# Optimization experiments

Measured on AMD Instinct MI355X. Metric: run time of the kernel, lower is better.

Reference implementation:

```python
import jax, jax.numpy as jnp
import numpy as np

B, L, D, H = 4, 2048, 2048, 16
HEAD_DIM = D // H
EPS = 1e-5


def rmsnorm(x, w):
    # fp32 RMSNorm as in the torch module
    xf = x.astype(jnp.float32)
    rms = jnp.sqrt(jnp.mean(xf * xf, axis=-1, keepdims=True) + EPS)
    return xf / rms * w


def apply_rope(x, freqs):
    # x: (..., D) with interleaved even/odd pairs; freqs: (2, L, D/2) = (sin, cos)
    sin, cos = freqs[0], freqs[1]
    xr = x.reshape(*x.shape[:-1], D // 2, 2)
    x_even, x_odd = xr[..., 0], xr[..., 1]
    e = x_even * cos - x_odd * sin
    o = x_odd * cos + x_even * sin
    return jnp.stack([e, o], axis=-1).reshape(x.shape)


def setup_inputs() -> dict:
    key = jax.random.key(0)
    k0, k1, k2 = jax.random.split(key, 3)
    x_BLD = jax.random.normal(k0, (B, L, D), dtype=jnp.float32)
    # realistic RoPE angle table over the full dim (matches module usage)
    t = jnp.arange(L, dtype=jnp.float32)[:, None]
    inv_freq = 1.0 / (10000.0 ** (jnp.arange(D // 2, dtype=jnp.float32) / (D // 2)))
    ang = t * inv_freq[None, :]                      # (L, D/2)
    freqs = jnp.stack([jnp.sin(ang), jnp.cos(ang)])  # (2, L, D/2)
    wqkv = jax.random.normal(k1, (3 * D, D), dtype=jnp.float32) * 0.02
    wo = jax.random.normal(k2, (D, D), dtype=jnp.float32) * 0.02
    q_norm_w = jnp.ones((D,), dtype=jnp.float32)
    k_norm_w = jnp.ones((D,), dtype=jnp.float32)
    return {"x_BLD": x_BLD, "freqs": freqs, "wqkv": wqkv, "wo": wo,
            "q_norm_w": q_norm_w, "k_norm_w": k_norm_w}


def reference(x_BLD, freqs, wqkv, wo, q_norm_w, k_norm_w):
    dtype = x_BLD.dtype
    qkv = x_BLD @ wqkv.T                             # (B, L, 3D)
    q, k, v = jnp.split(qkv, 3, axis=-1)
    q = apply_rope(rmsnorm(q, q_norm_w), freqs).astype(dtype)
    k = apply_rope(rmsnorm(k, k_norm_w), freqs).astype(dtype)
    # (B, L, D) -> (B, H, L, hd)
    q = q.reshape(B, L, H, HEAD_DIM).transpose(0, 2, 1, 3)
    k = k.reshape(B, L, H, HEAD_DIM).transpose(0, 2, 1, 3)
    v = v.reshape(B, L, H, HEAD_DIM).transpose(0, 2, 1, 3)
    scale = HEAD_DIM ** -0.5
    scores = jnp.einsum('bhqd,bhkd->bhqk', q, k) * scale
    attn = jax.nn.softmax(scores, axis=-1)
    out = jnp.einsum('bhqk,bhkd->bhqd', attn, v)
    out = out.transpose(0, 2, 1, 3).reshape(B, L, D)
    return out @ wo.T
```

## Files before the change

### kernel.cpp

```cpp
#include <hip/hip_runtime.h>
#include <stdint.h>
#include <stddef.h>

typedef unsigned short u16;
typedef __bf16 bf16x8 __attribute__((ext_vector_type(8)));
typedef float  f32x4  __attribute__((ext_vector_type(4)));
typedef float  f32x16 __attribute__((ext_vector_type(16)));

__device__ __forceinline__ float bf2f(u16 u){ return __uint_as_float(((unsigned)u)<<16); }
__device__ __forceinline__ u16 f2bf(float f){
  unsigned u = __float_as_uint(f);
  return (u16)((u + 0x7fffu + ((u>>16)&1u)) >> 16);
}
__device__ __forceinline__ void gl_lds16(const void* g, void* s){
  __builtin_amdgcn_global_load_lds(
      (__attribute__((address_space(1))) void*)(void*)g,
      (__attribute__((address_space(3))) void*)s, 16, 0, 0);
}

__global__ void k_f2bf(const float* __restrict__ in, u16* __restrict__ out, int n4){
  int i = blockIdx.x*256 + threadIdx.x;
  if (i < n4){
    float4 v = ((const float4*)in)[i];
    ((ushort4*)out)[i] = make_ushort4(f2bf(v.x), f2bf(v.y), f2bf(v.z), f2bf(v.w));
  }
}

#define BAR()  do{ __asm__ __volatile__("" ::: "memory"); \
                   __builtin_amdgcn_s_barrier(); \
                   __asm__ __volatile__("" ::: "memory"); }while(0)
#define LGKM0() __asm__ __volatile__("s_waitcnt lgkmcnt(0)" ::: "memory")
#define VMC4()  __asm__ __volatile__("s_waitcnt vmcnt(4)" ::: "memory")
#define VMC0()  __asm__ __volatile__("s_waitcnt vmcnt(0)" ::: "memory")

#define STAGE_A(B_,H_,T_) do{ \
  const u16* _s = A + (size_t)(m0 + (H_)*128 + w16 + sr)*K + (T_)*64 + sc; \
  gl_lds16(_s,               &As[B_][H_][w16*64]); \
  gl_lds16(_s + (size_t)8*K, &As[B_][H_][(w16+8)*64]); }while(0)
#define STAGE_B(B_,H_,T_) do{ \
  const u16* _s = Bm + (size_t)(n0 + (H_)*128 + w16 + sr)*K + (T_)*64 + sc; \
  gl_lds16(_s,               &Bs[B_][H_][w16*64]); \
  gl_lds16(_s + (size_t)8*K, &Bs[B_][H_][(w16+8)*64]); }while(0)

#define RD_A(H_,B_) do{ \
  _Pragma("unroll") for (int mt=0; mt<4; ++mt){ \
    int r_ = wm*64 + mt*16 + l16; const u16* p_ = &As[B_][H_][r_*64]; \
    af[mt][0] = *(const bf16x8*)&p_[(( quad    ^ (r_&7))<<3)]; \
    af[mt][1] = *(const bf16x8*)&p_[(((quad+4) ^ (r_&7))<<3)]; } }while(0)
#define RD_B(H_,B_) do{ \
  _Pragma("unroll") for (int nt=0; nt<2; ++nt){ \
    int r_ = wn*32 + nt*16 + l16; const u16* p_ = &Bs[B_][H_][r_*64]; \
    bfr[nt][0] = *(const bf16x8*)&p_[(( quad    ^ (r_&7))<<3)]; \
    bfr[nt][1] = *(const bf16x8*)&p_[(((quad+4) ^ (r_&7))<<3)]; } }while(0)

#define MM(QM,QN) do{ \
  LGKM0(); \
  __builtin_amdgcn_s_setprio(1); \
  _Pragma("unroll") for (int k_=0;k_<2;++k_) \
    _Pragma("unroll") for (int mt=0;mt<4;++mt) \
      _Pragma("unroll") for (int nt=0;nt<2;++nt) \
        acc[QM][QN][mt][nt] = __builtin_amdgcn_mfma_f32_16x16x32_bf16( \
            af[mt][k_], bfr[nt][k_], acc[QM][QN][mt][nt], 0,0,0); \
  __builtin_amdgcn_s_setprio(0); }while(0)

template<int BF16OUT>
__global__ __launch_bounds__(512,2) void k_gemm256(const u16* __restrict__ A,
                                                   const u16* __restrict__ Bm,
                                                   void* __restrict__ Cout,
                                                   int M, int N, int K){
  __shared__ __align__(16) u16 As[2][2][128*64];
  __shared__ __align__(16) u16 Bs[2][2][128*64];
  const int tid = threadIdx.x, w = tid>>6, ln = tid&63;
  const int l16 = ln&15, quad = ln>>4;
  const int wm = w&1, wn = w>>1;
  const int w16 = w*16, sr = ln>>3;
  const int sc = ((ln&7) ^ sr) << 3;
  const int nbx = N>>8;
  const int nwg = nbx*(M>>8);
  const int lid = blockIdx.y*nbx + blockIdx.x;
  const int swz = (lid&7)*(nwg>>3) + (lid>>3);
  const int m0 = (swz/nbx)<<8, n0 = (swz%nbx)<<8;

  f32x4 acc[2][2][4][2];
  #pragma unroll
  for (int a=0;a<2;++a)
    #pragma unroll
    for (int b=0;b<2;++b)
      #pragma unroll
      for (int c=0;c<4;++c)
        #pragma unroll
        for (int d=0;d<2;++d){ acc[a][b][c][d][0]=0.f; acc[a][b][c][d][1]=0.f;
                               acc[a][b][c][d][2]=0.f; acc[a][b][c][d][3]=0.f; }
  bf16x8 af[4][2], bfr[2][2];

  STAGE_A(0,0,0); STAGE_B(0,0,0); STAGE_A(0,1,0); STAGE_B(0,1,0);
  STAGE_B(1,0,1); STAGE_A(1,1,1);
  VMC4(); BAR();

  const int niter = K>>7;
  for (int j=0; j<niter-1; ++j){
    const int t1 = 2*j+1;
    RD_A(0,0); RD_B(0,0); STAGE_A(1,0,t1);           BAR(); MM(0,0); BAR();
    RD_A(1,0);            STAGE_B(1,1,t1);           BAR(); MM(1,0); BAR();
    RD_B(1,0);            STAGE_B(0,0,t1+1);         BAR(); MM(1,1); BAR();
    RD_A(0,0);            STAGE_A(0,1,t1+1); VMC4(); BAR(); MM(0,1); BAR();
    RD_A(0,1); RD_B(0,1); STAGE_A(0,0,t1+1);         BAR(); MM(0,0); BAR();
    RD_A(1,1);            STAGE_B(0,1,t1+1);         BAR(); MM(1,0); BAR();
    RD_B(1,1);            STAGE_B(1,0,t1+2);         BAR(); MM(1,1); BAR();
    RD_A(0,1);            STAGE_A(1,1,t1+2); VMC4(); BAR(); MM(0,1); BAR();
  }
  {
    const int T1 = 2*niter-1;
    RD_A(0,0); RD_B(0,0); STAGE_A(1,0,T1);           BAR(); MM(0,0); BAR();
    RD_A(1,0);            STAGE_B(1,1,T1);           BAR(); MM(1,0); BAR();
    RD_B(1,0);                                       BAR(); MM(1,1); BAR();
    RD_A(0,0);                               VMC0(); BAR(); MM(0,1); BAR();
    RD_A(0,1); RD_B(0,1);                            BAR(); MM(0,0); BAR();
    RD_A(1,1);                                       BAR(); MM(1,0); BAR();
    RD_B(1,1);                                       BAR(); MM(1,1); BAR();
    RD_A(0,1);                                       BAR(); MM(0,1); BAR();
  }
  #pragma unroll
  for (int qm=0;qm<2;++qm)
    #pragma unroll
    for (int qn=0;qn<2;++qn)
      #pragma unroll
      for (int mt=0;mt<4;++mt)
        #pragma unroll
        for (int nt=0;nt<2;++nt)
          #pragma unroll
          for (int jj=0;jj<4;++jj){
            int row = m0 + qm*128 + wm*64 + mt*16 + quad*4 + jj;
            int col = n0 + qn*128 + wn*32 + nt*16 + l16;
            if (BF16OUT) ((u16*)Cout)[(size_t)row*N + col] = f2bf(acc[qm][qn][mt][nt][jj]);
            else         ((float*)Cout)[(size_t)row*N + col] = acc[qm][qn][mt][nt][jj];
          }
}

__global__ void k_prep_qk(const u16* __restrict__ qkv, const float* __restrict__ freqs,
                          const float* __restrict__ qw, const float* __restrict__ kw,
                          u16* __restrict__ Qo, u16* __restrict__ Ko){
  const int row = blockIdx.x;
  const int b = row >> 11, l = row & 2047;
  const int tid = threadIdx.x;
  const u16* qr = qkv + (size_t)row*6144;
  float qe[4], qo[4], ke[4], ko_[4];
  float sq = 0.f, sk = 0.f;
  #pragma unroll
  for (int it=0; it<4; ++it){
    int p = tid + it*256;
    ushort2 q2 = ((const ushort2*)qr)[p];
    ushort2 k2 = ((const ushort2*)(qr+2048))[p];
    qe[it]=bf2f(q2.x); qo[it]=bf2f(q2.y);
    ke[it]=bf2f(k2.x); ko_[it]=bf2f(k2.y);
    sq += qe[it]*qe[it] + qo[it]*qo[it];
    sk += ke[it]*ke[it] + ko_[it]*ko_[it];
  }
  #pragma unroll
  for (int off=32; off; off>>=1){ sq += __shfl_xor(sq, off); sk += __shfl_xor(sk, off); }
  __shared__ float red[8];
  if ((tid&63)==0){ red[tid>>6]=sq; red[4+(tid>>6)]=sk; }
  __syncthreads();
  sq = red[0]+red[1]+red[2]+red[3];
  sk = red[4]+red[5]+red[6]+red[7];
  const float rq = rsqrtf(sq*(1.f/2048.f) + 1e-5f);
  const float rk = rsqrtf(sk*(1.f/2048.f) + 1e-5f);
  const float QS = 0.08838834764831845f * 1.4426950408889634f;
  #pragma unroll
  for (int it=0; it<4; ++it){
    int p = tid + it*256;
    float sn = freqs[(size_t)l*1024 + p];
    float cs = freqs[2097152 + (size_t)l*1024 + p];
    float2 w2q = ((const float2*)qw)[p];
    float2 w2k = ((const float2*)kw)[p];
    int h = p>>6, dd2 = p&63;
    size_t o = ((size_t)(b*16+h)*2048 + l)*64 + dd2;
    float a = qe[it]*rq*w2q.x, c = qo[it]*rq*w2q.y;
    ((ushort2*)Qo)[o] = make_ushort2(f2bf((a*cs - c*sn)*QS), f2bf((c*cs + a*sn)*QS));
    a = ke[it]*rk*w2k.x; c = ko_[it]*rk*w2k.y;
    ((ushort2*)Ko)[o] = make_ushort2(f2bf(a*cs - c*sn), f2bf(c*cs + a*sn));
  }
}

__global__ void k_prep_v(const u16* __restrict__ qkv, u16* __restrict__ Vt){
  const int lt = blockIdx.x, bh = blockIdx.y;
  const int b = bh>>4, h = bh&15;
  __shared__ u16 tile[64][136];
  const int tid = threadIdx.x;
  #pragma unroll
  for (int it=0; it<32; ++it){
    int idx = it*256 + tid;
    int lo = idx >> 7, dd = idx & 127;
    tile[lo][dd] = qkv[(size_t)(b*2048 + lt*64 + lo)*6144 + 4096 + h*128 + dd];
  }
  __syncthreads();
  #pragma unroll
  for (int it=0; it<32; ++it){
    int idx = it*256 + tid;
    int dd = idx >> 6, lo = idx & 63;
    Vt[((size_t)bh*128 + dd)*2048 + lt*64 + lo] = tile[lo][dd];
  }
}

__global__ __launch_bounds__(256,2) void k_flash(const u16* __restrict__ Q,
                                                 const u16* __restrict__ Kg,
                                                 const u16* __restrict__ Vt,
                                                 u16* __restrict__ O){
  __shared__ __align__(16) u16 Kt[128*136];
  __shared__ __align__(16) u16 Vs[128*136];
  const int qt = blockIdx.x, bh = blockIdx.y;
  const int tid = threadIdx.x, w = tid>>6, ln = tid&63;
  const int l31 = ln&31, hi = ln>>5;
  const int b = bh>>4, h = bh&15;
  const size_t qkbase = (size_t)bh*(2048*128);

  const int srow = tid>>4, scol = tid&15;
  const u16* kgp = Kg + qkbase + (size_t)srow*128 + scol*8;
  const u16* vgp = Vt + (size_t)bh*(128*2048) + (size_t)srow*2048 + scol*8;
  u16* kld = &Kt[srow*136 + scol*8];
  u16* vld = &Vs[srow*136 + scol*8];

  bf16x8 qf[8];
  {
    const u16* qp = Q + qkbase + (size_t)(qt*128 + w*32 + l31)*128 + hi*8;
    #pragma unroll
    for (int kk=0; kk<8; ++kk) qf[kk] = *(const bf16x8*)(qp + kk*16);
  }

  f32x16 o[4];
  #pragma unroll
  for (int dt=0; dt<4; ++dt)
    #pragma unroll
    for (int r=0; r<16; ++r) o[dt][r] = 0.f;
  float l_ = 0.f;

  bf16x8 kreg[8], vreg[8];
  #pragma unroll
  for (int it=0; it<8; ++it) kreg[it] = *(const bf16x8*)(kgp + (size_t)it*16*128);
  #pragma unroll
  for (int it=0; it<8; ++it) vreg[it] = *(const bf16x8*)(vgp + (size_t)it*16*2048);

  union U4 { unsigned u[4]; bf16x8 v; };

  for (int kt=0; kt<16; ++kt){
    __syncthreads();
    #pragma unroll
    for (int it=0; it<8; ++it) *(bf16x8*)(kld + it*16*136) = kreg[it];
    #pragma unroll
    for (int it=0; it<8; ++it) *(bf16x8*)(vld + it*16*136) = vreg[it];
    __syncthreads();
    if (kt < 15){
      #pragma unroll
      for (int it=0; it<8; ++it)
        kreg[it] = *(const bf16x8*)(kgp + (size_t)(kt+1)*128*128 + (size_t)it*16*128);
      #pragma unroll
      for (int it=0; it<8; ++it)
        vreg[it] = *(const bf16x8*)(vgp + (kt+1)*128 + (size_t)it*16*2048);
    }
    f32x16 s[4];
    #pragma unroll
    for (int t=0;t<4;++t)
      #pragma unroll
      for (int r=0;r<16;++r) s[t][r] = 0.f;
    #pragma unroll
    for (int kk=0; kk<8; ++kk){
      #pragma unroll
      for (int t=0; t<4; ++t){
        bf16x8 a = *(const bf16x8*)&Kt[(t*32 + l31)*136 + kk*16 + hi*8];
        s[t] = __builtin_amdgcn_mfma_f32_32x32x16_bf16(a, qf[kk], s[t], 0,0,0);
      }
    }
    float rs = 0.f;
    bf16x8 bfrag[8];
    #pragma unroll
    for (int t=0;t<4;++t){
      unsigned pk[4][2];
      #pragma unroll
      for (int g=0;g<4;++g){
        float p0 = exp2f(s[t][g*4+0] - 8.0f);
        float p1 = exp2f(s[t][g*4+1] - 8.0f);
        float p2 = exp2f(s[t][g*4+2] - 8.0f);
        float p3 = exp2f(s[t][g*4+3] - 8.0f);
        rs += (p0+p1)+(p2+p3);
        pk[g][0] = (unsigned)f2bf(p0) | ((unsigned)f2bf(p1)<<16);
        pk[g][1] = (unsigned)f2bf(p2) | ((unsigned)f2bf(p3)<<16);
      }
      unsigned a0 = (unsigned)__shfl_xor((int)(hi ? pk[0][0] : pk[1][0]), 32);
      unsigned a1 = (unsigned)__shfl_xor((int)(hi ? pk[0][1] : pk[1][1]), 32);
      unsigned b0 = (unsigned)__shfl_xor((int)(hi ? pk[2][0] : pk[3][0]), 32);
      unsigned b1 = (unsigned)__shfl_xor((int)(hi ? pk[2][1] : pk[3][1]), 32);
      U4 u0, u1;
      u0.u[0] = hi ? a0       : pk[0][0];
      u0.u[1] = hi ? a1       : pk[0][1];
      u0.u[2] = hi ? pk[1][0] : a0;
      u0.u[3] = hi ? pk[1][1] : a1;
      u1.u[0] = hi ? b0       : pk[2][0];
      u1.u[1] = hi ? b1       : pk[2][1];
      u1.u[2] = hi ? pk[3][0] : b0;
      u1.u[3] = hi ? pk[3][1] : b1;
      bfrag[t*2+0] = u0.v;
      bfrag[t*2+1] = u1.v;
    }
    rs += __shfl_xor(rs, 32);
    l_ += rs;
    #pragma unroll
    for (int kk=0; kk<8; ++kk){
      #pragma unroll
      for (int dt=0; dt<4; ++dt){
        bf16x8 a = *(const bf16x8*)&Vs[(dt*32 + l31)*136 + kk*16 + hi*8];
        o[dt] = __builtin_amdgcn_mfma_f32_32x32x16_bf16(a, bfrag[kk], o[dt], 0,0,0);
      }
    }
  }
  const float inv = 1.f/l_;
  __syncthreads();
  #pragma unroll
  for (int dt=0;dt<4;++dt)
    #pragma unroll
    for (int g=0;g<4;++g)
      *(ushort4*)&Kt[(w*32+l31)*136 + dt*32 + g*8 + hi*4] =
        make_ushort4(f2bf(o[dt][g*4+0]*inv), f2bf(o[dt][g*4+1]*inv),
                     f2bf(o[dt][g*4+2]*inv), f2bf(o[dt][g*4+3]*inv));
  __syncthreads();
  #pragma unroll
  for (int it=0; it<8; ++it){
    int q = it*16 + srow;
    bf16x8 vv = *(const bf16x8*)&Kt[q*136 + scol*8];
    *(bf16x8*)&O[(size_t)(b*2048 + qt*128 + q)*2048 + h*128 + scol*8] = vv;
  }
}

extern "C" void kernel_launch(void* const* d_in, const int* in_sizes, int n_in,
                              void* d_out, int out_size, void* d_ws, size_t ws_size,
                              hipStream_t stream){
  const float* x     = (const float*)d_in[0];
  const float* freqs = (const float*)d_in[1];
  const float* wqkv  = (const float*)d_in[2];
  const float* wo    = (const float*)d_in[3];
  const float* qw    = (const float*)d_in[4];
  const float* kw    = (const float*)d_in[5];
  char* ws = (char*)d_ws;
  u16* xbf    = (u16*)(ws);
  u16* wqkvbf = (u16*)(ws + 33554432);
  u16* wobf   = (u16*)(ws + 58720256);
  u16* qkvbf  = (u16*)(ws + 67108864);
  u16* Qbf    = (u16*)(ws + 167772160);
  u16* Kbf    = (u16*)(ws + 201326592);
  u16* Vtbf   = (u16*)(ws + 234881024);
  u16* Abf    = qkvbf;
  float* out  = (float*)d_out;

  k_f2bf<<<16384,256,0,stream>>>(x,    xbf,    4194304);
  k_f2bf<<<12288,256,0,stream>>>(wqkv, wqkvbf, 3145728);
  k_f2bf<<< 4096,256,0,stream>>>(wo,   wobf,   1048576);
  k_gemm256<1><<<dim3(24,32),512,0,stream>>>(xbf, wqkvbf, qkvbf, 8192, 6144, 2048);
  k_prep_qk<<<8192,256,0,stream>>>(qkvbf, freqs, qw, kw, Qbf, Kbf);
  k_prep_v<<<dim3(32,64),256,0,stream>>>(qkvbf, Vtbf);
  k_flash<<<dim3(16,64),256,0,stream>>>(Qbf, Kbf, Vtbf, Abf);
  k_gemm256<0><<<dim3(8,32),512,0,stream>>>(Abf, wobf, out, 8192, 2048, 2048);
}
```

Measured before the change: 698.2 us.

## Drop per-phase trailing barriers and explicit LDS waits in bf16 GEMM pipeline

Removes the workgroup barrier after each MFMA phase, keeping one only after every fourth phase, where the vmcnt wait now sits. It also replaces the blanket lgkmcnt(0) wait with sched_barrier fences, so the compiler places the LDS waits itself. The aim is to cut barrier stalls between waves in the double-buffered GEMM main loop. The risk is an LDS read/write race if a stage overwrites a buffer another wave is still reading.

```diff
diff --git a/kernel.cpp b/kernel.cpp
--- a/kernel.cpp
+++ b/kernel.cpp
@@ -29,7 +29,6 @@
 #define BAR()  do{ __asm__ __volatile__("" ::: "memory"); \
                    __builtin_amdgcn_s_barrier(); \
                    __asm__ __volatile__("" ::: "memory"); }while(0)
-#define LGKM0() __asm__ __volatile__("s_waitcnt lgkmcnt(0)" ::: "memory")
 #define VMC4()  __asm__ __volatile__("s_waitcnt vmcnt(4)" ::: "memory")
 #define VMC0()  __asm__ __volatile__("s_waitcnt vmcnt(0)" ::: "memory")
 
@@ -54,14 +53,15 @@
     bfr[nt][1] = *(const bf16x8*)&p_[(((quad+4) ^ (r_&7))<<3)]; } }while(0)
 
 #define MM(QM,QN) do{ \
-  LGKM0(); \
+  __builtin_amdgcn_sched_barrier(0); \
   __builtin_amdgcn_s_setprio(1); \
   _Pragma("unroll") for (int k_=0;k_<2;++k_) \
     _Pragma("unroll") for (int mt=0;mt<4;++mt) \
       _Pragma("unroll") for (int nt=0;nt<2;++nt) \
         acc[QM][QN][mt][nt] = __builtin_amdgcn_mfma_f32_16x16x32_bf16( \
             af[mt][k_], bfr[nt][k_], acc[QM][QN][mt][nt], 0,0,0); \
-  __builtin_amdgcn_s_setprio(0); }while(0)
+  __builtin_amdgcn_s_setprio(0); \
+  __builtin_amdgcn_sched_barrier(0); }while(0)
 
 template<int BF16OUT>
 __global__ __launch_bounds__(512,2) void k_gemm256(const u16* __restrict__ A,
@@ -100,25 +100,25 @@
   const int niter = K>>7;
   for (int j=0; j<niter-1; ++j){
     const int t1 = 2*j+1;
-    RD_A(0,0); RD_B(0,0); STAGE_A(1,0,t1);           BAR(); MM(0,0); BAR();
-    RD_A(1,0);            STAGE_B(1,1,t1);           BAR(); MM(1,0); BAR();
-    RD_B(1,0);            STAGE_B(0,0,t1+1);         BAR(); MM(1,1); BAR();
-    RD_A(0,0);            STAGE_A(0,1,t1+1); VMC4(); BAR(); MM(0,1); BAR();
-    RD_A(0,1); RD_B(0,1); STAGE_A(0,0,t1+1);         BAR(); MM(0,0); BAR();
-    RD_A(1,1);            STAGE_B(0,1,t1+1);         BAR(); MM(1,0); BAR();
-    RD_B(1,1);            STAGE_B(1,0,t1+2);         BAR(); MM(1,1); BAR();
-    RD_A(0,1);            STAGE_A(1,1,t1+2); VMC4(); BAR(); MM(0,1); BAR();
+    RD_A(0,0); RD_B(0,0); STAGE_A(1,0,t1);   BAR(); MM(0,0);
+    RD_A(1,0);            STAGE_B(1,1,t1);   BAR(); MM(1,0);
+    RD_B(1,0);            STAGE_B(0,0,t1+1); BAR(); MM(1,1);
+    RD_A(0,0);            STAGE_A(0,1,t1+1); BAR(); MM(0,1); VMC4(); BAR();
+    RD_A(0,1); RD_B(0,1); STAGE_A(0,0,t1+1); BAR(); MM(0,0);
+    RD_A(1,1);            STAGE_B(0,1,t1+1); BAR(); MM(1,0);
+    RD_B(1,1);            STAGE_B(1,0,t1+2); BAR(); MM(1,1);
+    RD_A(0,1);            STAGE_A(1,1,t1+2); BAR(); MM(0,1); VMC4(); BAR();
   }
   {
     const int T1 = 2*niter-1;
-    RD_A(0,0); RD_B(0,0); STAGE_A(1,0,T1);           BAR(); MM(0,0); BAR();
-    RD_A(1,0);            STAGE_B(1,1,T1);           BAR(); MM(1,0); BAR();
-    RD_B(1,0);                                       BAR(); MM(1,1); BAR();
-    RD_A(0,0);                               VMC0(); BAR(); MM(0,1); BAR();
-    RD_A(0,1); RD_B(0,1);                            BAR(); MM(0,0); BAR();
-    RD_A(1,1);                                       BAR(); MM(1,0); BAR();
-    RD_B(1,1);                                       BAR(); MM(1,1); BAR();
-    RD_A(0,1);                                       BAR(); MM(0,1); BAR();
+    RD_A(0,0); RD_B(0,0); STAGE_A(1,0,T1);   BAR(); MM(0,0);
+    RD_A(1,0);            STAGE_B(1,1,T1);   BAR(); MM(1,0);
+    RD_B(1,0);                               BAR(); MM(1,1);
+    RD_A(0,0);                               BAR(); MM(0,1); VMC0(); BAR();
+    RD_A(0,1); RD_B(0,1);                    BAR(); MM(0,0);
+    RD_A(1,1);                               BAR(); MM(1,0);
+    RD_B(1,1);                               BAR(); MM(1,1);
+    RD_A(0,1);                               BAR(); MM(0,1);
   }
   #pragma unroll
   for (int qm=0;qm<2;++qm)
```

Measured after the change: 682.3 us. 1.02x faster.
